# Optimization experiments

Hardware: AMD Instinct MI355X
Metric: run time of the kernel (lower is better)

Reference implementation:

```python
import jax, jax.numpy as jnp
import numpy as np

B, S, D, H, E = 8, 2048, 1024, 4096, 8


def setup_inputs() -> dict:
    key = jax.random.key(0)
    k0, k1, k2, k3 = jax.random.split(key, 4)
    x = jax.random.normal(k0, (B, S, D), dtype=jnp.float32)
    # hash-router assignment: one expert per token, shape [B, S, 1] (top-k dim k=1)
    assign = jax.random.randint(k1, (B, S, 1), 0, E, dtype=jnp.int64)
    # per-expert Linear(dim, hidden): W_e [E, D, H], b_e [E, H]
    W_e = jax.random.normal(k2, (E, D, H), dtype=jnp.float32) * (1.0 / np.sqrt(D))
    b_e = jnp.zeros((E, H), dtype=jnp.float32)
    # shared output Linear(hidden, dim)
    W_out = jax.random.normal(k3, (H, D), dtype=jnp.float32) * (1.0 / np.sqrt(H))
    b_out = jnp.zeros((D,), dtype=jnp.float32)
    return {"x": x, "W_e": W_e, "b_e": b_e, "W_out": W_out, "b_out": b_out,
            "assign": assign}


def reference(x, W_e, b_e, W_out, b_out, assign):
    num_experts = W_e.shape[0]
    hidden = W_e.shape[2]
    # zero-init combine buffer, matching torch.zeros(batch, seq, hidden)
    expert_out = jnp.zeros(x.shape[:2] + (hidden,), dtype=x.dtype)
    for e in range(num_experts):  # fixed small expert loop
        y = jnp.einsum("bsd,dh->bsh", x, W_e[e]) + b_e[e]
        mask = (assign == e).any(-1)  # [B, S]
        expert_out = jnp.where(mask[..., None], y, expert_out)
    h = jax.nn.relu(expert_out)
    return jnp.einsum("bsh,hd->bsd", h, W_out) + b_out
```

## Files before the change

kernel.cpp:

```cpp
#include <hip/hip_runtime.h>
#include <hip/hip_bf16.h>
#include <stdint.h>

#define NB 8
#define NS 2048
#define ND 1024
#define NH 4096
#define NE 8
#define NTOK (NB*NS)

typedef __bf16 bf16;
typedef bf16 bf16x8 __attribute__((ext_vector_type(8)));
typedef float f32x4 __attribute__((ext_vector_type(4)));

static const size_t OFF_XB  = 128 * 1024;
static const size_t OFF_WTE = OFF_XB  + (size_t)NTOK * ND * 2;
static const size_t OFF_WTO = OFF_WTE + (size_t)NE * NH * ND * 2;
static const size_t OFF_HB  = OFF_WTO + (size_t)ND * NH * 2;
static const size_t WS_NEED = OFF_HB  + (size_t)NTOK * NH * 2;

#define GLDS16(src, dst) __builtin_amdgcn_global_load_lds( \
    (__attribute__((address_space(1))) void*)(void*)(src), \
    (__attribute__((address_space(3))) void*)(dst), 16, 0, 0)


__global__ void k_hist(const int* __restrict__ assign, int* __restrict__ meta) {
    int t = blockIdx.x * blockDim.x + threadIdx.x;
    if (t < NTOK) atomicAdd(&meta[assign[t] & 7], 1);
}

__global__ void k_desc(int* __restrict__ meta) {
    int lane = threadIdx.x;
    int counts[NE], offs[NE + 1];
    offs[0] = 0;
#pragma unroll
    for (int e = 0; e < NE; e++) { counts[e] = meta[e]; offs[e + 1] = offs[e] + counts[e]; }
    if (lane < NE + 1) meta[16 + lane] = offs[lane];
    int base[NE];
    int nt = 0;
#pragma unroll
    for (int e = 0; e < NE; e++) { base[e] = nt; nt += (counts[e] + 255) >> 8; }
    if (lane == 0) meta[25] = nt;
    for (int t = lane; t < nt; t += 64) {
        int e = 0;
#pragma unroll
        for (int k = 1; k < NE; k++) if (t >= base[k]) e = k;
        int t0 = (t - base[e]) << 8;
        meta[32 + t] = e;
        meta[128 + t] = offs[e] + t0;
        meta[256 + t] = min(256, counts[e] - t0);
    }
}

__global__ void k_scatter(const int* __restrict__ assign, int* __restrict__ meta) {
    int t = blockIdx.x * blockDim.x + threadIdx.x;
    if (t < NTOK) {
        int e = assign[t] & 7;
        int p = atomicAdd(&meta[8 + e], 1);
        int* perm = meta + 512;
        perm[meta[16 + e] + p] = t;
    }
}

__global__ void k_gather_cvt(const float* __restrict__ x, const int* __restrict__ meta,
                             bf16* __restrict__ xbp) {
    long i = (long)blockIdx.x * blockDim.x + threadIdx.x;
    int row = (int)(i >> 7);
    int c8  = (int)(i & 127);
    const int* perm = meta + 512;
    int tok = perm[row];
    const float4* s = (const float4*)(x + (size_t)tok * ND + c8 * 8);
    float4 v0 = s[0], v1 = s[1];
    bf16x8 o;
    o[0] = (bf16)v0.x; o[1] = (bf16)v0.y; o[2] = (bf16)v0.z; o[3] = (bf16)v0.w;
    o[4] = (bf16)v1.x; o[5] = (bf16)v1.y; o[6] = (bf16)v1.z; o[7] = (bf16)v1.w;
    *(bf16x8*)(xbp + i * 8) = o;
}

__global__ void k_transpose(const float* __restrict__ in, bf16* __restrict__ out,
                            int R, int C) {
    __shared__ float tile[32][33];
    int b  = blockIdx.z;
    int c0 = blockIdx.x * 32, r0 = blockIdx.y * 32;
    const float* inb = in + (size_t)b * R * C;
    bf16* outb = out + (size_t)b * R * C;
    int tx = threadIdx.x, ty = threadIdx.y;
#pragma unroll
    for (int i = 0; i < 4; i++) {
        int r = r0 + ty + i * 8;
        tile[ty + i * 8][tx] = inb[(size_t)r * C + c0 + tx];
    }
    __syncthreads();
#pragma unroll
    for (int i = 0; i < 4; i++) {
        int c = c0 + ty + i * 8;
        outb[(size_t)c * R + r0 + tx] = (bf16)tile[tx][ty + i * 8];
    }
}


#define BAR { __builtin_amdgcn_s_barrier(); asm volatile("" ::: "memory"); }
#define VMC4 asm volatile("s_waitcnt vmcnt(4)" ::: "memory")
#define VMC0 asm volatile("s_waitcnt vmcnt(0)" ::: "memory")

#define LDA(msub) { \
  const char* Ab = sm + dbuf + wr * 16384; \
  _Pragma("unroll") for (int m = 0; m < 4; m++) { \
    int row = ((msub) * 4 + m) * 16 + lr; \
    af[m][0] = *(const bf16x8*)(Ab + row * 128 + xk0); \
    af[m][1] = *(const bf16x8*)(Ab + row * 128 + xk1); \
  } }

#define LDB(nsub) { \
  const char* Bb = sm + dbuf + 32768 + (wc >> 1) * 16384; \
  _Pragma("unroll") for (int n = 0; n < 2; n++) { \
    int row = (wc & 1) * 64 + ((nsub) * 2 + n) * 16 + lr; \
    bfr[(nsub)*2+n][0] = *(const bf16x8*)(Bb + row * 128 + xk0); \
    bfr[(nsub)*2+n][1] = *(const bf16x8*)(Bb + row * 128 + xk1); \
  } }

#define MFMA_Q(msub, nsub) { \
  __builtin_amdgcn_s_setprio(1); \
  _Pragma("unroll") for (int m = 0; m < 4; m++) \
  _Pragma("unroll") for (int n = 0; n < 2; n++) \
  _Pragma("unroll") for (int k = 0; k < 2; k++) \
    acc[(msub)*4+m][(nsub)*2+n] = __builtin_amdgcn_mfma_f32_16x16x32_bf16( \
        af[m][k], bfr[(nsub)*2+n][k], acc[(msub)*4+m][(nsub)*2+n], 0, 0, 0); \
  __builtin_amdgcn_s_setprio(0); }

#define DO_TILE(i, S0, S1, S2, S3, VW) { \
  const int dbuf = ((i) & 1) * 65536; \
  LDA(0); LDB(0); S0; BAR; MFMA_Q(0,0); BAR; \
  LDB(1);         S1; BAR; MFMA_Q(0,1); BAR; \
  LDA(1);         S2; BAR; MFMA_Q(1,0); BAR; \
                  S3; VW; BAR; MFMA_Q(1,1); BAR; \
}

__launch_bounds__(512, 2)
__global__ void k_gemm1(const bf16* __restrict__ xbp, const bf16* __restrict__ wte,
                        const float* __restrict__ b_e, bf16* __restrict__ hb,
                        const int* __restrict__ meta) {
    __shared__ __align__(16) char sm[2 * 65536];
    int nt = meta[25];
    int f = blockIdx.x;
    int xcd = f & 7, j = f >> 3;
    int bx = j & 15, tslot = j >> 4;
    int tileIdx = xcd + 8 * tslot;
    if (tileIdx >= nt) return;
    int e  = meta[32 + tileIdx];
    int rs = meta[128 + tileIdx];
    int rc = meta[256 + tileIdx];
    int n0 = bx * 256;

    int tid = threadIdx.x;
    int lane = tid & 63, wid = tid >> 6;
    int wr = wid >> 2, wc = wid & 3;
    int lr = lane & 15, kg = lane >> 4;
    int xk0 = (kg ^ (lr & 7)) * 16;
    int xk1 = ((4 + kg) ^ (lr & 7)) * 16;

    int sr = tid >> 3, sl = tid & 7;
    int g = sl ^ (sr & 7);
    const bf16* pa[2][2];
#pragma unroll
    for (int h = 0; h < 2; h++)
#pragma unroll
      for (int r = 0; r < 2; r++) {
        int arow = h * 128 + r * 64 + sr;
        int p = rs + (arow < rc - 1 ? arow : rc - 1);
        pa[h][r] = xbp + (size_t)p * ND + g * 8;
      }
    const bf16* pb0 = wte + ((size_t)e * NH + n0 + sr) * ND + g * 8;

#define STAGE_A(t, h) { \
    char* d = sm + ((t) & 1) * 65536 + (h) * 16384 + wid * 1024; \
    GLDS16(pa[h][0] + (size_t)(t) * 64, d); \
    GLDS16(pa[h][1] + (size_t)(t) * 64, d + 8192); }
#define STAGE_B(t, h) { \
    char* d = sm + ((t) & 1) * 65536 + 32768 + (h) * 16384 + wid * 1024; \
    GLDS16(pb0 + ((h) * 128) * (size_t)ND + (size_t)(t) * 64, d); \
    GLDS16(pb0 + ((h) * 128 + 64) * (size_t)ND + (size_t)(t) * 64, d + 8192); }

    f32x4 acc[8][4] = {};
    bf16x8 af[4][2], bfr[4][2];
    const int NT = ND / 64;

    STAGE_B(0, 0); STAGE_B(0, 1); STAGE_A(0, 0); STAGE_A(0, 1);
    STAGE_B(1, 0); STAGE_B(1, 1);
    VMC4;
    BAR;

#pragma unroll 2
    for (int i = 0; i < NT - 2; i++)
        DO_TILE(i, STAGE_A(i + 1, 0), STAGE_A(i + 1, 1),
                   STAGE_B(i + 2, 0), STAGE_B(i + 2, 1), VMC4);
    DO_TILE(NT - 2, STAGE_A(NT - 1, 0), STAGE_A(NT - 1, 1), , , VMC0);
    DO_TILE(NT - 1, , , , , );

    float bias[4];
#pragma unroll
    for (int n = 0; n < 4; n++) bias[n] = b_e[e * NH + n0 + wc * 64 + n * 16 + lr];
#pragma unroll
    for (int m = 0; m < 8; m++) {
#pragma unroll
        for (int r = 0; r < 4; r++) {
            int row = wr * 128 + m * 16 + kg * 4 + r;
            if (row < rc) {
                bf16* hp = hb + (size_t)(rs + row) * NH + n0 + wc * 64;
#pragma unroll
                for (int n = 0; n < 4; n++)
                    hp[n * 16 + lr] = (bf16)fmaxf(acc[m][n][r] + bias[n], 0.0f);
            }
        }
    }
#undef STAGE_A
#undef STAGE_B
}

__launch_bounds__(512, 2)
__global__ void k_gemm2(const bf16* __restrict__ hb, const bf16* __restrict__ wto,
                        const float* __restrict__ b_out, const int* __restrict__ meta,
                        float* __restrict__ out) {
    __shared__ __align__(16) char sm[2 * 65536];
    int lin = blockIdx.x;
    int swz = (lin & 7) * 32 + (lin >> 3);
    int bx = swz & 3, by = swz >> 2;
    int m0 = by * 256, n0 = bx * 256;
    const int* perm = meta + 512;

    int tid = threadIdx.x;
    int lane = tid & 63, wid = tid >> 6;
    int wr = wid >> 2, wc = wid & 3;
    int lr = lane & 15, kg = lane >> 4;
    int xk0 = (kg ^ (lr & 7)) * 16;
    int xk1 = ((4 + kg) ^ (lr & 7)) * 16;

    int sr = tid >> 3, sl = tid & 7;
    int g = sl ^ (sr & 7);
    const bf16* pa0 = hb  + ((size_t)m0 + sr) * NH + g * 8;
    const bf16* pb0 = wto + ((size_t)n0 + sr) * NH + g * 8;

#define STAGE_A(t, h) { \
    char* d = sm + ((t) & 1) * 65536 + (h) * 16384 + wid * 1024; \
    GLDS16(pa0 + ((h) * 128) * (size_t)NH + (size_t)(t) * 64, d); \
    GLDS16(pa0 + ((h) * 128 + 64) * (size_t)NH + (size_t)(t) * 64, d + 8192); }
#define STAGE_B(t, h) { \
    char* d = sm + ((t) & 1) * 65536 + 32768 + (h) * 16384 + wid * 1024; \
    GLDS16(pb0 + ((h) * 128) * (size_t)NH + (size_t)(t) * 64, d); \
    GLDS16(pb0 + ((h) * 128 + 64) * (size_t)NH + (size_t)(t) * 64, d + 8192); }

    f32x4 acc[8][4] = {};
    bf16x8 af[4][2], bfr[4][2];
    const int NT = NH / 64;

    STAGE_B(0, 0); STAGE_B(0, 1); STAGE_A(0, 0); STAGE_A(0, 1);
    STAGE_B(1, 0); STAGE_B(1, 1);
    VMC4;
    BAR;

#pragma unroll 2
    for (int i = 0; i < NT - 2; i++)
        DO_TILE(i, STAGE_A(i + 1, 0), STAGE_A(i + 1, 1),
                   STAGE_B(i + 2, 0), STAGE_B(i + 2, 1), VMC4);
    DO_TILE(NT - 2, STAGE_A(NT - 1, 0), STAGE_A(NT - 1, 1), , , VMC0);
    DO_TILE(NT - 1, , , , , );

    float bias[4];
#pragma unroll
    for (int n = 0; n < 4; n++) bias[n] = b_out[n0 + wc * 64 + n * 16 + lr];
#pragma unroll
    for (int m = 0; m < 8; m++) {
#pragma unroll
        for (int r = 0; r < 4; r++) {
            int prow = m0 + wr * 128 + m * 16 + kg * 4 + r;
            int tok = perm[prow];
            float* op = out + (size_t)tok * ND + n0 + wc * 64;
#pragma unroll
            for (int n = 0; n < 4; n++)
                op[n * 16 + lr] = acc[m][n][r] + bias[n];
        }
    }
#undef STAGE_A
#undef STAGE_B
}

extern "C" void kernel_launch(void* const* d_in, const int* in_sizes, int n_in,
                              void* d_out, int out_size, void* d_ws, size_t ws_size,
                              hipStream_t stream) {
    const float* x     = (const float*)d_in[0];
    const float* W_e   = (const float*)d_in[1];
    const float* b_e   = (const float*)d_in[2];
    const float* W_out = (const float*)d_in[3];
    const float* b_out = (const float*)d_in[4];
    const int*   assign = (const int*)d_in[5];
    float* out = (float*)d_out;

    if (ws_size < WS_NEED) return;

    char* ws = (char*)d_ws;
    int*  meta = (int*)ws;
    bf16* xbp = (bf16*)(ws + OFF_XB);
    bf16* wte = (bf16*)(ws + OFF_WTE);
    bf16* wto = (bf16*)(ws + OFF_WTO);
    bf16* hb  = (bf16*)(ws + OFF_HB);

    hipMemsetAsync(meta, 0, 512 * sizeof(int), stream);

    k_hist<<<NTOK / 256, 256, 0, stream>>>(assign, meta);
    k_desc<<<1, 64, 0, stream>>>(meta);
    k_scatter<<<NTOK / 256, 256, 0, stream>>>(assign, meta);
    k_gather_cvt<<<NTOK * ND / (256 * 8), 256, 0, stream>>>(x, meta, xbp);
    k_transpose<<<dim3(NH / 32, ND / 32, NE), dim3(32, 8), 0, stream>>>(W_e, wte, ND, NH);
    k_transpose<<<dim3(ND / 32, NH / 32, 1), dim3(32, 8), 0, stream>>>(W_out, wto, NH, ND);
    k_gemm1<<<1152, 512, 0, stream>>>(xbp, wte, b_e, hb, meta);
    k_gemm2<<<256, 512, 0, stream>>>(hb, wto, b_out, meta, out);
}
```

Before: 490.9 us.

## Triple-buffer A tiles in LDS and fuse routing into one kernel

Both GEMMs move from double-buffered A/B tiles to a triple-buffered A ring plus a double-buffered B, using 160 KB of LDS. This lets A tiles be prefetched two steps ahead and wait on a deeper vmcnt, hiding more global-load latency; the loop is also unrolled further. The memset and the histogram/descriptor/scatter kernels are replaced by a single-block routing kernel that uses shared-memory atomics. GEMM1 now derives its expert and row range directly from the block index, mapping one expert per XCD. The single-block router serializes routing on one CU, and the larger LDS footprint limits occupancy.

```diff
diff --git a/kernel.cpp b/kernel.cpp
--- a/kernel.cpp
+++ b/kernel.cpp
@@ -24,41 +24,28 @@
     (__attribute__((address_space(3))) void*)(dst), 16, 0, 0)
 
 
-__global__ void k_hist(const int* __restrict__ assign, int* __restrict__ meta) {
-    int t = blockIdx.x * blockDim.x + threadIdx.x;
-    if (t < NTOK) atomicAdd(&meta[assign[t] & 7], 1);
-}
-
-__global__ void k_desc(int* __restrict__ meta) {
-    int lane = threadIdx.x;
-    int counts[NE], offs[NE + 1];
-    offs[0] = 0;
-#pragma unroll
-    for (int e = 0; e < NE; e++) { counts[e] = meta[e]; offs[e + 1] = offs[e] + counts[e]; }
-    if (lane < NE + 1) meta[16 + lane] = offs[lane];
-    int base[NE];
-    int nt = 0;
-#pragma unroll
-    for (int e = 0; e < NE; e++) { base[e] = nt; nt += (counts[e] + 255) >> 8; }
-    if (lane == 0) meta[25] = nt;
-    for (int t = lane; t < nt; t += 64) {
-        int e = 0;
-#pragma unroll
-        for (int k = 1; k < NE; k++) if (t >= base[k]) e = k;
-        int t0 = (t - base[e]) << 8;
-        meta[32 + t] = e;
-        meta[128 + t] = offs[e] + t0;
-        meta[256 + t] = min(256, counts[e] - t0);
-    }
-}
-
-__global__ void k_scatter(const int* __restrict__ assign, int* __restrict__ meta) {
-    int t = blockIdx.x * blockDim.x + threadIdx.x;
-    if (t < NTOK) {
+__global__ void k_route(const int* __restrict__ assign, int* __restrict__ meta) {
+    __shared__ int cnt[NE];
+    __shared__ int offs_s[NE];
+    int tid = threadIdx.x;
+    if (tid < NE) cnt[tid] = 0;
+    __syncthreads();
+    for (int t = tid; t < NTOK; t += 1024) atomicAdd(&cnt[assign[t] & 7], 1);
+    __syncthreads();
+    if (tid == 0) {
+        int o = 0;
+        for (int e = 0; e < NE; e++) {
+            meta[e] = cnt[e]; meta[16 + e] = o; offs_s[e] = o; o += cnt[e];
+        }
+    }
+    __syncthreads();
+    if (tid < NE) cnt[tid] = offs_s[tid];
+    __syncthreads();
+    int* perm = meta + 512;
+    for (int t = tid; t < NTOK; t += 1024) {
         int e = assign[t] & 7;
-        int p = atomicAdd(&meta[8 + e], 1);
-        int* perm = meta + 512;
-        perm[meta[16 + e] + p] = t;
+        int p = atomicAdd(&cnt[e], 1);
+        perm[p] = t;
     }
 }
 
@@ -100,11 +87,11 @@
 
 
 #define BAR { __builtin_amdgcn_s_barrier(); asm volatile("" ::: "memory"); }
-#define VMC4 asm volatile("s_waitcnt vmcnt(4)" ::: "memory")
+#define VMC8 asm volatile("s_waitcnt vmcnt(8)" ::: "memory")
 #define VMC0 asm volatile("s_waitcnt vmcnt(0)" ::: "memory")
 
 #define LDA(msub) { \
-  const char* Ab = sm + dbuf + wr * 16384; \
+  const char* Ab = sm + abuf + wr * 16384; \
   _Pragma("unroll") for (int m = 0; m < 4; m++) { \
     int row = ((msub) * 4 + m) * 16 + lr; \
     af[m][0] = *(const bf16x8*)(Ab + row * 128 + xk0); \
@@ -112,7 +99,7 @@
   } }
 
 #define LDB(nsub) { \
-  const char* Bb = sm + dbuf + 32768 + (wc >> 1) * 16384; \
+  const char* Bb = sm + bbuf + (wc >> 1) * 16384; \
   _Pragma("unroll") for (int n = 0; n < 2; n++) { \
     int row = (wc & 1) * 64 + ((nsub) * 2 + n) * 16 + lr; \
     bfr[(nsub)*2+n][0] = *(const bf16x8*)(Bb + row * 128 + xk0); \
@@ -129,27 +116,35 @@
   __builtin_amdgcn_s_setprio(0); }
 
 #define DO_TILE(i, S0, S1, S2, S3, VW) { \
-  const int dbuf = ((i) & 1) * 65536; \
+  const int abuf = ((i) % 3) * 32768; \
+  const int bbuf = 98304 + ((i) & 1) * 32768; \
   LDA(0); LDB(0); S0; BAR; MFMA_Q(0,0); BAR; \
   LDB(1);         S1; BAR; MFMA_Q(0,1); BAR; \
   LDA(1);         S2; BAR; MFMA_Q(1,0); BAR; \
                   S3; VW; BAR; MFMA_Q(1,1); BAR; \
 }
 
+#define STAGE_A(t, h) { \
+    char* d = sm + ((t) % 3) * 32768 + (h) * 16384 + wid * 1024; \
+    GLDS16(srcA(t, h, 0), d); \
+    GLDS16(srcA(t, h, 1), d + 8192); }
+#define STAGE_B(t, h) { \
+    char* d = sm + 98304 + ((t) & 1) * 32768 + (h) * 16384 + wid * 1024; \
+    GLDS16(srcB(t, h, 0), d); \
+    GLDS16(srcB(t, h, 1), d + 8192); }
+
 __launch_bounds__(512, 2)
 __global__ void k_gemm1(const bf16* __restrict__ xbp, const bf16* __restrict__ wte,
                         const float* __restrict__ b_e, bf16* __restrict__ hb,
                         const int* __restrict__ meta) {
-    __shared__ __align__(16) char sm[2 * 65536];
-    int nt = meta[25];
+    __shared__ __align__(16) char sm[163840];
     int f = blockIdx.x;
-    int xcd = f & 7, j = f >> 3;
-    int bx = j & 15, tslot = j >> 4;
-    int tileIdx = xcd + 8 * tslot;
-    if (tileIdx >= nt) return;
-    int e  = meta[32 + tileIdx];
-    int rs = meta[128 + tileIdx];
-    int rc = meta[256 + tileIdx];
+    int e = f & 7, r2 = f >> 3;
+    int bx = r2 & 15, j = r2 >> 4;
+    int cnt = meta[e];
+    int rs  = meta[16 + e] + j * 256;
+    int rc  = cnt - j * 256; if (rc > 256) rc = 256;
+    if (rc <= 0) return;
     int n0 = bx * 256;
 
     int tid = threadIdx.x;
@@ -165,36 +160,30 @@
 #pragma unroll
     for (int h = 0; h < 2; h++)
 #pragma unroll
-      for (int r = 0; r < 2; r++) {
-        int arow = h * 128 + r * 64 + sr;
+      for (int rr = 0; rr < 2; rr++) {
+        int arow = h * 128 + rr * 64 + sr;
         int p = rs + (arow < rc - 1 ? arow : rc - 1);
-        pa[h][r] = xbp + (size_t)p * ND + g * 8;
+        pa[h][rr] = xbp + (size_t)p * ND + g * 8;
       }
     const bf16* pb0 = wte + ((size_t)e * NH + n0 + sr) * ND + g * 8;
 
-#define STAGE_A(t, h) { \
-    char* d = sm + ((t) & 1) * 65536 + (h) * 16384 + wid * 1024; \
-    GLDS16(pa[h][0] + (size_t)(t) * 64, d); \
-    GLDS16(pa[h][1] + (size_t)(t) * 64, d + 8192); }
-#define STAGE_B(t, h) { \
-    char* d = sm + ((t) & 1) * 65536 + 32768 + (h) * 16384 + wid * 1024; \
-    GLDS16(pb0 + ((h) * 128) * (size_t)ND + (size_t)(t) * 64, d); \
-    GLDS16(pb0 + ((h) * 128 + 64) * (size_t)ND + (size_t)(t) * 64, d + 8192); }
+#define srcA(t, h, rr) (pa[h][rr] + (size_t)(t) * 64)
+#define srcB(t, h, rr) (pb0 + ((h) * 128 + (rr) * 64) * (size_t)ND + (size_t)(t) * 64)
 
     f32x4 acc[8][4] = {};
     bf16x8 af[4][2], bfr[4][2];
     const int NT = ND / 64;
 
-    STAGE_B(0, 0); STAGE_B(0, 1); STAGE_A(0, 0); STAGE_A(0, 1);
-    STAGE_B(1, 0); STAGE_B(1, 1);
-    VMC4;
+    STAGE_A(0, 0); STAGE_A(0, 1); STAGE_B(0, 0); STAGE_B(0, 1);
+    STAGE_A(1, 0); STAGE_A(1, 1); STAGE_B(1, 0); STAGE_B(1, 1);
+    VMC8;
     BAR;
 
-#pragma unroll 2
+#pragma unroll 6
     for (int i = 0; i < NT - 2; i++)
-        DO_TILE(i, STAGE_A(i + 1, 0), STAGE_A(i + 1, 1),
-                   STAGE_B(i + 2, 0), STAGE_B(i + 2, 1), VMC4);
-    DO_TILE(NT - 2, STAGE_A(NT - 1, 0), STAGE_A(NT - 1, 1), , , VMC0);
+        DO_TILE(i, STAGE_A(i + 2, 0), STAGE_A(i + 2, 1),
+                   STAGE_B(i + 2, 0), STAGE_B(i + 2, 1), VMC8);
+    DO_TILE(NT - 2, , , , , VMC0);
     DO_TILE(NT - 1, , , , , );
 
     float bias[4];
@@ -203,25 +192,25 @@
 #pragma unroll
     for (int m = 0; m < 8; m++) {
 #pragma unroll
-        for (int r = 0; r < 4; r++) {
-            int row = wr * 128 + m * 16 + kg * 4 + r;
+        for (int rr = 0; rr < 4; rr++) {
+            int row = wr * 128 + m * 16 + kg * 4 + rr;
             if (row < rc) {
                 bf16* hp = hb + (size_t)(rs + row) * NH + n0 + wc * 64;
 #pragma unroll
                 for (int n = 0; n < 4; n++)
-                    hp[n * 16 + lr] = (bf16)fmaxf(acc[m][n][r] + bias[n], 0.0f);
+                    hp[n * 16 + lr] = (bf16)fmaxf(acc[m][n][rr] + bias[n], 0.0f);
             }
         }
     }
-#undef STAGE_A
-#undef STAGE_B
+#undef srcA
+#undef srcB
 }
 
 __launch_bounds__(512, 2)
 __global__ void k_gemm2(const bf16* __restrict__ hb, const bf16* __restrict__ wto,
                         const float* __restrict__ b_out, const int* __restrict__ meta,
                         float* __restrict__ out) {
-    __shared__ __align__(16) char sm[2 * 65536];
+    __shared__ __align__(16) char sm[163840];
     int lin = blockIdx.x;
     int swz = (lin & 7) * 32 + (lin >> 3);
     int bx = swz & 3, by = swz >> 2;
@@ -240,29 +229,23 @@
     const bf16* pa0 = hb  + ((size_t)m0 + sr) * NH + g * 8;
     const bf16* pb0 = wto + ((size_t)n0 + sr) * NH + g * 8;
 
-#define STAGE_A(t, h) { \
-    char* d = sm + ((t) & 1) * 65536 + (h) * 16384 + wid * 1024; \
-    GLDS16(pa0 + ((h) * 128) * (size_t)NH + (size_t)(t) * 64, d); \
-    GLDS16(pa0 + ((h) * 128 + 64) * (size_t)NH + (size_t)(t) * 64, d + 8192); }
-#define STAGE_B(t, h) { \
-    char* d = sm + ((t) & 1) * 65536 + 32768 + (h) * 16384 + wid * 1024; \
-    GLDS16(pb0 + ((h) * 128) * (size_t)NH + (size_t)(t) * 64, d); \
-    GLDS16(pb0 + ((h) * 128 + 64) * (size_t)NH + (size_t)(t) * 64, d + 8192); }
+#define srcA(t, h, rr) (pa0 + ((h) * 128 + (rr) * 64) * (size_t)NH + (size_t)(t) * 64)
+#define srcB(t, h, rr) (pb0 + ((h) * 128 + (rr) * 64) * (size_t)NH + (size_t)(t) * 64)
 
     f32x4 acc[8][4] = {};
     bf16x8 af[4][2], bfr[4][2];
     const int NT = NH / 64;
 
-    STAGE_B(0, 0); STAGE_B(0, 1); STAGE_A(0, 0); STAGE_A(0, 1);
-    STAGE_B(1, 0); STAGE_B(1, 1);
-    VMC4;
+    STAGE_A(0, 0); STAGE_A(0, 1); STAGE_B(0, 0); STAGE_B(0, 1);
+    STAGE_A(1, 0); STAGE_A(1, 1); STAGE_B(1, 0); STAGE_B(1, 1);
+    VMC8;
     BAR;
 
-#pragma unroll 2
+#pragma unroll 6
     for (int i = 0; i < NT - 2; i++)
-        DO_TILE(i, STAGE_A(i + 1, 0), STAGE_A(i + 1, 1),
-                   STAGE_B(i + 2, 0), STAGE_B(i + 2, 1), VMC4);
-    DO_TILE(NT - 2, STAGE_A(NT - 1, 0), STAGE_A(NT - 1, 1), , , VMC0);
+        DO_TILE(i, STAGE_A(i + 2, 0), STAGE_A(i + 2, 1),
+                   STAGE_B(i + 2, 0), STAGE_B(i + 2, 1), VMC8);
+    DO_TILE(NT - 2, , , , , VMC0);
     DO_TILE(NT - 1, , , , , );
 
     float bias[4];
@@ -271,17 +254,17 @@
 #pragma unroll
     for (int m = 0; m < 8; m++) {
 #pragma unroll
-        for (int r = 0; r < 4; r++) {
-            int prow = m0 + wr * 128 + m * 16 + kg * 4 + r;
+        for (int rr = 0; rr < 4; rr++) {
+            int prow = m0 + wr * 128 + m * 16 + kg * 4 + rr;
             int tok = perm[prow];
             float* op = out + (size_t)tok * ND + n0 + wc * 64;
 #pragma unroll
             for (int n = 0; n < 4; n++)
-                op[n * 16 + lr] = acc[m][n][r] + bias[n];
+                op[n * 16 + lr] = acc[m][n][rr] + bias[n];
         }
     }
-#undef STAGE_A
-#undef STAGE_B
+#undef srcA
+#undef srcB
 }
 
 extern "C" void kernel_launch(void* const* d_in, const int* in_sizes, int n_in,
@@ -304,11 +287,7 @@
     bf16* wto = (bf16*)(ws + OFF_WTO);
     bf16* hb  = (bf16*)(ws + OFF_HB);
 
-    hipMemsetAsync(meta, 0, 512 * sizeof(int), stream);
-
-    k_hist<<<NTOK / 256, 256, 0, stream>>>(assign, meta);
-    k_desc<<<1, 64, 0, stream>>>(meta);
-    k_scatter<<<NTOK / 256, 256, 0, stream>>>(assign, meta);
+    k_route<<<1, 1024, 0, stream>>>(assign, meta);
     k_gather_cvt<<<NTOK * ND / (256 * 8), 256, 0, stream>>>(x, meta, xbp);
     k_transpose<<<dim3(NH / 32, ND / 32, NE), dim3(32, 8), 0, stream>>>(W_e, wte, ND, NH);
     k_transpose<<<dim3(ND / 32, NH / 32, 1), dim3(32, 8), 0, stream>>>(W_out, wto, NH, ND);
```

Result: faster. 443.1 us (-9.7%).
